# Kernel optimization log

Measured on AMD Instinct MI355X. Metric: run time of the kernel, lower is better.

## Reference

```python
import jax, jax.numpy as jnp
from jax import lax
import numpy as np

TAU = 10.0      # tauSr == tauRef
THR = 1.0       # theta
WIDTH = 1.0     # tauRho (surrogate width)
SCALE = 1.0     # scaleRho (surrogate scale)
DECAY = float(np.exp(-1.0 / TAU))


@jax.custom_vjp
def _heaviside(v):
    # spike = 1[v >= theta]
    return (v >= THR).astype(v.dtype)

def _heaviside_fwd(v):
    return _heaviside(v), v

def _heaviside_bwd(v, g):
    # SLAYER exponential surrogate pdf: scaleRho/tauRho * exp(-|v-theta|/tauRho)
    return (g * (SCALE / WIDTH) * jnp.exp(-jnp.abs(v - THR) / WIDTH),)

_heaviside.defvjp(_heaviside_fwd, _heaviside_bwd)


def _conv2d(x, w, pad):
    # x: (B, Cin, H, W), w: (Cout, Cin, kh, kw); SLAYER convs have no bias
    return lax.conv_general_dilated(
        x, w, window_strides=(1, 1), padding=[(pad, pad), (pad, pad)],
        dimension_numbers=("NCHW", "OIHW", "NCHW"))


def _sumpool(x, k):
    # SLAYER pool = sum over kxk window (times a learned scalar applied outside)
    B, C, H, W = x.shape
    return x.reshape(B, C, H // k, k, W // k, k).sum(axis=(3, 5))


def _psp(seq):
    # exponential synaptic (PSP) filter along time: s[t] = a*s[t-1] + x[t]
    a = jnp.asarray(DECAY, seq.dtype)
    def step(s, x_t):
        s = a * s + x_t
        return s, s
    _, out = lax.scan(step, jnp.zeros_like(seq[0]), seq)
    return out  # (T, ...)


def _spikes(u):
    # thresholded spiking with decaying refractory feedback (scaleRef=1):
    # v[t] = u[t] - r[t]; s[t] = 1[v >= theta]; r[t+1] = b*(r[t] + theta*s[t])
    b = jnp.asarray(DECAY, u.dtype)
    def step(r, u_t):
        s = _heaviside(u_t - r)
        r_next = b * (r + THR * s)
        return r_next, s
    _, out = lax.scan(step, jnp.zeros_like(u[0]), u)
    return out  # (T, ...)


def _forward(x, conv1_w, conv2_w, lin_w, w_pool1, w_pool2):
    N, T, C, H, W = x.shape  # (64, 100, 2, 32, 32)
    h = _conv2d(x.reshape(N * T, C, H, W), conv1_w, 2)        # (NT, 4, 32, 32)
    h = _sumpool(h, 4) * w_pool1                               # (NT, 4, 8, 8)
    h = h.reshape(N, T, 4, 8, 8).swapaxes(0, 1)                # (T, N, 4, 8, 8)
    s1 = _spikes(_psp(h))                                      # (T, N, 4, 8, 8)
    h2 = _conv2d(s1.reshape(T * N, 4, 8, 8), conv2_w, 1)       # (TN, 8, 8, 8)
    h2 = (_sumpool(h2, 2) * w_pool2).reshape(T, N, 8, 4, 4)    # (T, N, 8, 4, 4)
    s2 = _spikes(_psp(h2))                                     # (T, N, 8, 4, 4)
    # dense = full-spatial conv (2, 8, 4, 4) -> (N, T, 2)
    return jnp.einsum("tnchw,ochw->nto", s2, lin_w)


def setup_inputs() -> dict:
    key = jax.random.key(0)
    ks = jax.random.split(key, 4)
    x = (jax.random.uniform(ks[0], (64, 100, 2, 32, 32)) < 0.1).astype(jnp.float32)
    conv1_w = jax.random.normal(ks[1], (4, 2, 5, 5), jnp.float32) * 0.3
    conv2_w = jax.random.normal(ks[2], (8, 4, 3, 3), jnp.float32) * 0.3
    lin_w = jax.random.normal(ks[3], (2, 8, 4, 4), jnp.float32) * 0.3
    w_pool1 = jnp.float32(1.0 / 16.0)  # 1.1*theta / (16 * 1.1)
    w_pool2 = jnp.float32(1.0 / 4.0)   # 1.1*theta / (4 * 1.1)
    return {"x": x, "conv1_w": conv1_w, "conv2_w": conv2_w, "lin_w": lin_w,
            "w_pool1": w_pool1, "w_pool2": w_pool2}


def reference(x, conv1_w, conv2_w, lin_w, w_pool1, w_pool2):
    return _forward(x, conv1_w, conv2_w, lin_w, w_pool1, w_pool2)
```

## Files before the change

### kernel.cpp

```cpp
#include <hip/hip_runtime.h>


#define DECAY 0.9048374180359595f

#define BAR_LGKM() asm volatile("s_waitcnt lgkmcnt(0)\n\ts_barrier" ::: "memory")
#define FENCE_LGKM() asm volatile("s_waitcnt lgkmcnt(0)" ::: "memory")

typedef __attribute__((ext_vector_type(8))) _Float16 half8;

__global__ __launch_bounds__(128) void k0_fold(const float* __restrict__ w1,
        const float* __restrict__ w2, const float* __restrict__ wp1,
        const float* __restrict__ wp2, float* __restrict__ wl1,
        float* __restrict__ wl2, float* __restrict__ out) {
    const int tid = threadIdx.x;
    out[blockIdx.x * 128 + tid] = 0.f;
    if (blockIdx.x != 0) return;
    const float p1 = wp1[0], p2 = wp2[0];
    for (int idx = tid; idx < 512; idx += 128) {
        const int f = idx & 7, c = (idx >> 3) & 3, e = (idx >> 5) & 7, cin = idx >> 8;
        const int cc = c * 2 + cin;
        int alo = e - 3; if (alo < 0) alo = 0;
        int ahi = e;     if (ahi > 4) ahi = 4;
        int blo = f - 3; if (blo < 0) blo = 0;
        int bhi = f;     if (bhi > 4) bhi = 4;
        float s = 0.f;
        for (int a = alo; a <= ahi; ++a)
            for (int b = blo; b <= bhi; ++b)
                s += w1[cc * 25 + a * 5 + b];
        wl1[(cin * 8 + e) * 32 + c * 8 + f] = s * p1;
    }
    for (int idx = tid; idx < 512; idx += 128) {
        const int c2 = idx & 7, f = (idx >> 3) & 3, e = (idx >> 5) & 3, cin = idx >> 7;
        int alo = e - 1; if (alo < 0) alo = 0;
        int ahi = e;     if (ahi > 2) ahi = 2;
        int blo = f - 1; if (blo < 0) blo = 0;
        int bhi = f;     if (bhi > 2) bhi = 2;
        float s = 0.f;
        for (int aa = alo; aa <= ahi; ++aa)
            for (int bb = blo; bb <= bhi; ++bb)
                s += w2[((c2 * 4 + cin) * 3 + aa) * 3 + bb];
        wl2[c2 * 68 + cin * 16 + e * 4 + f] = s * p2;
    }
}

__global__ __launch_bounds__(64) void k1(const float* __restrict__ x,
        const float* __restrict__ wg, float* __restrict__ u1) {
    __shared__ __align__(16) float xs[2 * 1296];
    __shared__ __align__(16) float wl[512];
    const int lane = threadIdx.x;
    const int frame = blockIdx.x;
    const int n = frame / 100, t = frame % 100;

    *(float4*)(wl + 4 * lane)       = *(const float4*)(wg + 4 * lane);
    *(float4*)(wl + 256 + 4 * lane) = *(const float4*)(wg + 256 + 4 * lane);

    #pragma unroll
    for (int m0 = 0; m0 < 128; m0 += 64) {
        const int m = m0 + lane;
        if (m < 72) {
            const int cin = m / 36, rem = m % 36;
            const int rr = rem / 9, q4 = rem % 9;
            const int pr = (rr == 0) ? 0 : (rr == 1) ? 9 : (rr == 2) ? 26 : 35;
            *(float4*)(xs + cin * 1296 + pr * 36 + q4 * 4) = make_float4(0.f, 0.f, 0.f, 0.f);
        }
    }
    #pragma unroll
    for (int m0 = 0; m0 < 192; m0 += 64) {
        const int m = m0 + lane;
        if (m < 144) {
            const int cin = m / 72, rem = m % 72;
            const int side = rem & 1, pr = rem >> 1;
            *(float2*)(xs + cin * 1296 + pr * 36 + side * 34) = make_float2(0.f, 0.f);
        }
    }
    const float4* xg = (const float4*)(x + (size_t)frame * 2048);
    #pragma unroll
    for (int q = 0; q < 8; ++q) {
        const int m = q * 64 + lane;
        const float4 v = xg[m];
        const int li = 4 * m;
        const int cin = li >> 10, row = (li >> 5) & 31, col = li & 31;
        const int r = row + 2;
        const int pr = (r & 3) * 9 + (r >> 2);
        float* d = xs + cin * 1296 + pr * 36 + col + 2;
        *(float2*)(d)     = make_float2(v.x, v.y);
        *(float2*)(d + 2) = make_float2(v.z, v.w);
    }
    FENCE_LGKM();

    const int cp = lane >> 5;
    const int i  = (lane >> 2) & 7;
    const int jh = (lane >> 1) & 1;
    const int eh = lane & 1;

    float acc[2][4] = {{0.f, 0.f, 0.f, 0.f}, {0.f, 0.f, 0.f, 0.f}};
    const float* tb = xs + (i + eh) * 36 + jh * 16;
    #pragma unroll
    for (int cin = 0; cin < 2; ++cin) {
        #pragma unroll
        for (int et = 0; et < 4; ++et) {
            const int ro = cin * 1296 + et * 9 * 36;
            float xr[20];
            #pragma unroll
            for (int b = 0; b < 5; ++b)
                *(float4*)(xr + 4 * b) = *(const float4*)(tb + ro + 4 * b);
            float wv[16];
            const float* wp = wl + (cin * 8 + eh * 4 + et) * 32 + cp * 16;
            #pragma unroll
            for (int q = 0; q < 4; ++q)
                *(float4*)(wv + 4 * q) = *(const float4*)(wp + 4 * q);
            #pragma unroll
            for (int cl = 0; cl < 2; ++cl) {
                #pragma unroll
                for (int jj = 0; jj < 4; ++jj) {
                    const int o = 4 * jj;
                    acc[cl][jj] += xr[o]*wv[cl*8]     + xr[o+1]*wv[cl*8+1]
                                 + xr[o+2]*wv[cl*8+2] + xr[o+3]*wv[cl*8+3]
                                 + xr[o+4]*wv[cl*8+4] + xr[o+5]*wv[cl*8+5]
                                 + xr[o+6]*wv[cl*8+6] + xr[o+7]*wv[cl*8+7];
                }
            }
        }
    }
    #pragma unroll
    for (int cl = 0; cl < 2; ++cl)
        #pragma unroll
        for (int jj = 0; jj < 4; ++jj)
            acc[cl][jj] += __shfl_xor(acc[cl][jj], 1);

    const float o0 = eh ? acc[1][0] : acc[0][0];
    const float o1 = eh ? acc[1][1] : acc[0][1];
    const float o2 = eh ? acc[1][2] : acc[0][2];
    const float o3 = eh ? acc[1][3] : acc[0][3];
    *(float4*)(u1 + (size_t)t * 16384 + n * 256 + (2 * cp + eh) * 64 + i * 8 + jh * 4) =
        make_float4(o0, o1, o2, o3);
}

__global__ __launch_bounds__(256, 2) void kf(const float* __restrict__ u1,
        const float* __restrict__ wl2g, const float* __restrict__ lw,
        float* __restrict__ out) {
    __shared__ __align__(16) _Float16 ls1h[100 * 264];
    __shared__ __align__(16) float    ls2[100 * 20];
    const int tid = threadIdx.x;
    const int bid = blockIdx.x;
    const int n   = (bid & 7) * 8 + (bid >> 6);
    const int oct = (bid >> 3) & 7;
    const int wave = tid >> 6, l64 = tid & 63;
    const float a = DECAY;

    const float* up = u1 + n * 256 + tid;

    const int sub = tid >> 3, l8 = tid & 7;
    const int i2 = l8 >> 1, jhp = l8 & 1;

    float4 wreg[16];
    {
        const float* wbase = wl2g + oct * 68;
        #pragma unroll
        for (int q = 0; q < 16; ++q)
            wreg[q] = *(const float4*)(wbase + (q >> 2) * 16 + (q & 3) * 4);
    }

    float vbuf[100];
    #pragma unroll
    for (int k = 0; k < 100; ++k) vbuf[k] = up[(size_t)k * 16384];
    {
        float psp = 0.f, rr = 0.f;
        #pragma unroll
        for (int k = 0; k < 100; ++k) {
            psp = a * psp + vbuf[k];
            const float vv = psp - rr;
            const float s = (vv >= 1.f) ? 1.f : 0.f;
            rr = a * (rr + s);
            ls1h[k * 264 + tid] = (_Float16)s;
        }
    }
    BAR_LGKM();

    #pragma unroll 1
    for (int pass = 0; pass < 4; ++pass) {
        const int slot = sub + 32 * pass;
        if (slot < 100) {
            const _Float16* sb = ls1h + slot * 264;
            float acc0 = 0.f, acc1 = 0.f;
            #pragma unroll
            for (int cin = 0; cin < 4; ++cin) {
                #pragma unroll
                for (int e = 0; e < 4; ++e) {
                    const int ri = 2 * i2 + e - 1;
                    const int rc = (ri < 0) ? 0 : (ri > 7 ? 7 : ri);
                    const bool rok = (ri >= 0) && (ri <= 7);
                    const half8 hv = *(const half8*)(sb + cin * 64 + rc * 8);
                    float rr8[8];
                    #pragma unroll
                    for (int m = 0; m < 8; ++m) rr8[m] = (float)hv[m];
                    float xr[6];
                    xr[0] = jhp ? rr8[3] : 0.0f;
                    xr[1] = jhp ? rr8[4] : rr8[0];
                    xr[2] = jhp ? rr8[5] : rr8[1];
                    xr[3] = jhp ? rr8[6] : rr8[2];
                    xr[4] = jhp ? rr8[7] : rr8[3];
                    xr[5] = jhp ? 0.0f   : rr8[4];
                    if (!rok) {
                        #pragma unroll
                        for (int m = 0; m < 6; ++m) xr[m] = 0.0f;
                    }
                    const float4 wf = wreg[cin * 4 + e];
                    acc0 += xr[0] * wf.x; acc0 += xr[1] * wf.y;
                    acc0 += xr[2] * wf.z; acc0 += xr[3] * wf.w;
                    acc1 += xr[2] * wf.x; acc1 += xr[3] * wf.y;
                    acc1 += xr[4] * wf.z; acc1 += xr[5] * wf.w;
                }
            }
            *(float2*)(ls2 + slot * 20 + i2 * 4 + 2 * jhp) =
                make_float2(acc0, acc1);
        }
    }
    BAR_LGKM();

    if (wave == 0 && l64 < 16) {
        float ub[100];
        #pragma unroll
        for (int k = 0; k < 100; ++k) ub[k] = ls2[k * 20 + l64];
        float psp2 = 0.f, rr2 = 0.f;
        #pragma unroll
        for (int k = 0; k < 100; ++k) {
            psp2 = a * psp2 + ub[k];
            const float vv = psp2 - rr2;
            const float s = (vv >= 1.f) ? 1.f : 0.f;
            rr2 = a * (rr2 + s);
            ls2[k * 20 + l64] = s;
        }
    }
    BAR_LGKM();

    if (tid < 200) {
        const int t = tid >> 1, o = tid & 1;
        const float* srow = ls2 + t * 20;
        const float* wrow = lw + o * 128 + oct * 16;
        const float4 s0 = *(const float4*)(srow);
        const float4 s1 = *(const float4*)(srow + 4);
        const float4 s2 = *(const float4*)(srow + 8);
        const float4 s3 = *(const float4*)(srow + 12);
        const float4 w0 = *(const float4*)(wrow);
        const float4 w1 = *(const float4*)(wrow + 4);
        const float4 w2 = *(const float4*)(wrow + 8);
        const float4 w3 = *(const float4*)(wrow + 12);
        float v = 0.f;
        v += s0.x * w0.x; v += s0.y * w0.y; v += s0.z * w0.z; v += s0.w * w0.w;
        v += s1.x * w1.x; v += s1.y * w1.y; v += s1.z * w1.z; v += s1.w * w1.w;
        v += s2.x * w2.x; v += s2.y * w2.y; v += s2.z * w2.z; v += s2.w * w2.w;
        v += s3.x * w3.x; v += s3.y * w3.y; v += s3.z * w3.z; v += s3.w * w3.w;
        atomicAdd(&out[n * 200 + t * 2 + o], v);
    }
}

extern "C" void kernel_launch(void* const* d_in, const int* in_sizes, int n_in,
                              void* d_out, int out_size, void* d_ws, size_t ws_size,
                              hipStream_t stream) {
    const float* x   = (const float*)d_in[0];
    const float* w1  = (const float*)d_in[1];
    const float* w2  = (const float*)d_in[2];
    const float* lw  = (const float*)d_in[3];
    const float* wp1 = (const float*)d_in[4];
    const float* wp2 = (const float*)d_in[5];

    float* u1  = (float*)d_ws;
    float* wl1 = u1 + 1638400;
    float* wl2 = wl1 + 512;
    float* out = (float*)d_out;

    k0_fold<<<100, 128, 0, stream>>>(w1, w2, wp1, wp2, wl1, wl2, out);
    k1<<<6400, 64, 0, stream>>>(x, wl1, u1);
    kf<<<512, 256, 0, stream>>>(u1, wl2, lw, out);
}
```

Baseline: 117.6 us.

## Fuse weight folding, conv1 and recurrent stages into one cooperative kernel

Merges the three launches (weight fold, per-frame conv1, and the spiking/conv2/dense stage) into a single cooperative kernel of 512 blocks, separated by a grid-wide sync. Each block recomputes the folded conv1 and conv2 weights locally in shared memory, and its four waves each process one frame per pass over four passes. This removes launch overhead and the global workspace round trip for folded weights. In exchange it adds a grid barrier, caps the grid at 512 blocks for the conv1 phase, and raises shared memory use, which may limit occupancy.

Result: slower. 194.1 us (+65.0%).

```diff
diff --git a/kernel.cpp b/kernel.cpp
--- a/kernel.cpp
+++ b/kernel.cpp
@@ -1,4 +1,7 @@
 #include <hip/hip_runtime.h>
+#include <hip/hip_cooperative_groups.h>
+
+namespace cg = cooperative_groups;
 
 
 #define DECAY 0.9048374180359595f
@@ -8,29 +11,146 @@
 
 typedef __attribute__((ext_vector_type(8))) _Float16 half8;
 
-__global__ __launch_bounds__(128) void k0_fold(const float* __restrict__ w1,
-        const float* __restrict__ w2, const float* __restrict__ wp1,
-        const float* __restrict__ wp2, float* __restrict__ wl1,
-        float* __restrict__ wl2, float* __restrict__ out) {
-    const int tid = threadIdx.x;
-    out[blockIdx.x * 128 + tid] = 0.f;
-    if (blockIdx.x != 0) return;
-    const float p1 = wp1[0], p2 = wp2[0];
-    for (int idx = tid; idx < 512; idx += 128) {
-        const int f = idx & 7, c = (idx >> 3) & 3, e = (idx >> 5) & 7, cin = idx >> 8;
-        const int cc = c * 2 + cin;
-        int alo = e - 3; if (alo < 0) alo = 0;
-        int ahi = e;     if (ahi > 4) ahi = 4;
-        int blo = f - 3; if (blo < 0) blo = 0;
-        int bhi = f;     if (bhi > 4) bhi = 4;
-        float s = 0.f;
-        for (int a = alo; a <= ahi; ++a)
-            for (int b = blo; b <= bhi; ++b)
-                s += w1[cc * 25 + a * 5 + b];
-        wl1[(cin * 8 + e) * 32 + c * 8 + f] = s * p1;
-    }
-    for (int idx = tid; idx < 512; idx += 128) {
-        const int c2 = idx & 7, f = (idx >> 3) & 3, e = (idx >> 5) & 3, cin = idx >> 7;
+__global__ __launch_bounds__(256, 2) void kall(
+        const float* __restrict__ x,   const float* __restrict__ w1,
+        const float* __restrict__ w2,  const float* __restrict__ lw,
+        const float* __restrict__ wp1, const float* __restrict__ wp2,
+        float* __restrict__ u1,        float* __restrict__ out) {
+    __shared__ __align__(16) char smem[60800];
+    float*    xs_all = (float*)smem;
+    float*    wl1s   = (float*)(smem + 41472);
+    float*    w1s    = (float*)(smem + 43520);
+    _Float16* ls1h   = (_Float16*)smem;
+    float*    ls2    = (float*)(smem + 52800);
+
+    const int tid  = threadIdx.x;
+    const int bid  = blockIdx.x;
+    const int wave = tid >> 6, lane = tid & 63;
+    const float a = DECAY;
+
+    if (bid < 50) out[bid * 256 + tid] = 0.f;
+    if (tid < 200) w1s[tid] = w1[tid];
+    __syncthreads();
+    {
+        const float p1 = wp1[0];
+        #pragma unroll
+        for (int rep = 0; rep < 2; ++rep) {
+            const int idx = rep * 256 + tid;
+            const int f = idx & 7, c = (idx >> 3) & 3, e = (idx >> 5) & 7, cin = idx >> 8;
+            const int cc = c * 2 + cin;
+            int alo = e - 3; if (alo < 0) alo = 0;
+            int ahi = e;     if (ahi > 4) ahi = 4;
+            int blo = f - 3; if (blo < 0) blo = 0;
+            int bhi = f;     if (bhi > 4) bhi = 4;
+            float s = 0.f;
+            for (int aa = alo; aa <= ahi; ++aa)
+                for (int bb = blo; bb <= bhi; ++bb)
+                    s += w1s[cc * 25 + aa * 5 + bb];
+            wl1s[(cin * 8 + e) * 32 + c * 8 + f] = s * p1;
+        }
+    }
+    __syncthreads();
+
+    float* xs = xs_all + wave * 2592;
+    #pragma unroll 1
+    for (int pass = 0; pass < 4; ++pass) {
+        const int frame = pass * 2048 + bid * 4 + wave;
+        if (frame < 6400) {
+            const int n = frame / 100, t = frame % 100;
+
+            #pragma unroll
+            for (int m0 = 0; m0 < 128; m0 += 64) {
+                const int m = m0 + lane;
+                if (m < 72) {
+                    const int cin = m / 36, rem = m % 36;
+                    const int rr = rem / 9, q4 = rem % 9;
+                    const int pr = (rr == 0) ? 0 : (rr == 1) ? 9 : (rr == 2) ? 26 : 35;
+                    *(float4*)(xs + cin * 1296 + pr * 36 + q4 * 4) =
+                        make_float4(0.f, 0.f, 0.f, 0.f);
+                }
+            }
+            #pragma unroll
+            for (int m0 = 0; m0 < 192; m0 += 64) {
+                const int m = m0 + lane;
+                if (m < 144) {
+                    const int cin = m / 72, rem = m % 72;
+                    const int side = rem & 1, pr = rem >> 1;
+                    *(float2*)(xs + cin * 1296 + pr * 36 + side * 34) =
+                        make_float2(0.f, 0.f);
+                }
+            }
+            const float4* xg = (const float4*)(x + (size_t)frame * 2048);
+            #pragma unroll
+            for (int q = 0; q < 8; ++q) {
+                const int m = q * 64 + lane;
+                const float4 v = xg[m];
+                const int li = 4 * m;
+                const int cin = li >> 10, row = (li >> 5) & 31, col = li & 31;
+                const int r = row + 2;
+                const int pr = (r & 3) * 9 + (r >> 2);
+                float* d = xs + cin * 1296 + pr * 36 + col + 2;
+                *(float2*)(d)     = make_float2(v.x, v.y);
+                *(float2*)(d + 2) = make_float2(v.z, v.w);
+            }
+            FENCE_LGKM();
+
+            const int cp = lane >> 5;
+            const int i  = (lane >> 2) & 7;
+            const int jh = (lane >> 1) & 1;
+            const int eh = lane & 1;
+
+            float acc[2][4] = {{0.f, 0.f, 0.f, 0.f}, {0.f, 0.f, 0.f, 0.f}};
+            const float* tb = xs + (i + eh) * 36 + jh * 16;
+            #pragma unroll
+            for (int cin = 0; cin < 2; ++cin) {
+                #pragma unroll
+                for (int et = 0; et < 4; ++et) {
+                    const int ro = cin * 1296 + et * 9 * 36;
+                    float xr[20];
+                    #pragma unroll
+                    for (int b = 0; b < 5; ++b)
+                        *(float4*)(xr + 4 * b) = *(const float4*)(tb + ro + 4 * b);
+                    float wv[16];
+                    const float* wp = wl1s + (cin * 8 + eh * 4 + et) * 32 + cp * 16;
+                    #pragma unroll
+                    for (int q = 0; q < 4; ++q)
+                        *(float4*)(wv + 4 * q) = *(const float4*)(wp + 4 * q);
+                    #pragma unroll
+                    for (int cl = 0; cl < 2; ++cl) {
+                        #pragma unroll
+                        for (int jj = 0; jj < 4; ++jj) {
+                            const int o = 4 * jj;
+                            acc[cl][jj] += xr[o]*wv[cl*8]     + xr[o+1]*wv[cl*8+1]
+                                         + xr[o+2]*wv[cl*8+2] + xr[o+3]*wv[cl*8+3]
+                                         + xr[o+4]*wv[cl*8+4] + xr[o+5]*wv[cl*8+5]
+                                         + xr[o+6]*wv[cl*8+6] + xr[o+7]*wv[cl*8+7];
+                        }
+                    }
+                }
+            }
+            #pragma unroll
+            for (int cl = 0; cl < 2; ++cl)
+                #pragma unroll
+                for (int jj = 0; jj < 4; ++jj)
+                    acc[cl][jj] += __shfl_xor(acc[cl][jj], 1);
+
+            const float o0 = eh ? acc[1][0] : acc[0][0];
+            const float o1 = eh ? acc[1][1] : acc[0][1];
+            const float o2 = eh ? acc[1][2] : acc[0][2];
+            const float o3 = eh ? acc[1][3] : acc[0][3];
+            *(float4*)(u1 + (size_t)t * 16384 + n * 256 + (2 * cp + eh) * 64 + i * 8 + jh * 4) =
+                make_float4(o0, o1, o2, o3);
+        }
+    }
+
+    cg::this_grid().sync();
+
+    const int nB  = (bid & 7) * 8 + (bid >> 6);
+    const int oct = (bid >> 3) & 7;
+
+    if (tid < 64) {
+        const float p2 = wp2[0];
+        const int cin = tid >> 4, e = (tid >> 2) & 3, f = tid & 3;
         int alo = e - 1; if (alo < 0) alo = 0;
         int ahi = e;     if (ahi > 2) ahi = 2;
         int blo = f - 1; if (blo < 0) blo = 0;
@@ -38,128 +158,20 @@
         float s = 0.f;
         for (int aa = alo; aa <= ahi; ++aa)
             for (int bb = blo; bb <= bhi; ++bb)
-                s += w2[((c2 * 4 + cin) * 3 + aa) * 3 + bb];
-        wl2[c2 * 68 + cin * 16 + e * 4 + f] = s * p2;
-    }
-}
-
-__global__ __launch_bounds__(64) void k1(const float* __restrict__ x,
-        const float* __restrict__ wg, float* __restrict__ u1) {
-    __shared__ __align__(16) float xs[2 * 1296];
-    __shared__ __align__(16) float wl[512];
-    const int lane = threadIdx.x;
-    const int frame = blockIdx.x;
-    const int n = frame / 100, t = frame % 100;
-
-    *(float4*)(wl + 4 * lane)       = *(const float4*)(wg + 4 * lane);
-    *(float4*)(wl + 256 + 4 * lane) = *(const float4*)(wg + 256 + 4 * lane);
-
+                s += w2[((oct * 4 + cin) * 3 + aa) * 3 + bb];
+        ls2[cin * 16 + e * 4 + f] = s * p2;
+    }
+    __syncthreads();
+
+    float4 wreg[16];
     #pragma unroll
-    for (int m0 = 0; m0 < 128; m0 += 64) {
-        const int m = m0 + lane;
-        if (m < 72) {
-            const int cin = m / 36, rem = m % 36;
-            const int rr = rem / 9, q4 = rem % 9;
-            const int pr = (rr == 0) ? 0 : (rr == 1) ? 9 : (rr == 2) ? 26 : 35;
-            *(float4*)(xs + cin * 1296 + pr * 36 + q4 * 4) = make_float4(0.f, 0.f, 0.f, 0.f);
-        }
-    }
-    #pragma unroll
-    for (int m0 = 0; m0 < 192; m0 += 64) {
-        const int m = m0 + lane;
-        if (m < 144) {
-            const int cin = m / 72, rem = m % 72;
-            const int side = rem & 1, pr = rem >> 1;
-            *(float2*)(xs + cin * 1296 + pr * 36 + side * 34) = make_float2(0.f, 0.f);
-        }
-    }
-    const float4* xg = (const float4*)(x + (size_t)frame * 2048);
-    #pragma unroll
-    for (int q = 0; q < 8; ++q) {
-        const int m = q * 64 + lane;
-        const float4 v = xg[m];
-        const int li = 4 * m;
-        const int cin = li >> 10, row = (li >> 5) & 31, col = li & 31;
-        const int r = row + 2;
-        const int pr = (r & 3) * 9 + (r >> 2);
-        float* d = xs + cin * 1296 + pr * 36 + col + 2;
-        *(float2*)(d)     = make_float2(v.x, v.y);
-        *(float2*)(d + 2) = make_float2(v.z, v.w);
-    }
-    FENCE_LGKM();
-
-    const int cp = lane >> 5;
-    const int i  = (lane >> 2) & 7;
-    const int jh = (lane >> 1) & 1;
-    const int eh = lane & 1;
-
-    float acc[2][4] = {{0.f, 0.f, 0.f, 0.f}, {0.f, 0.f, 0.f, 0.f}};
-    const float* tb = xs + (i + eh) * 36 + jh * 16;
-    #pragma unroll
-    for (int cin = 0; cin < 2; ++cin) {
-        #pragma unroll
-        for (int et = 0; et < 4; ++et) {
-            const int ro = cin * 1296 + et * 9 * 36;
-            float xr[20];
-            #pragma unroll
-            for (int b = 0; b < 5; ++b)
-                *(float4*)(xr + 4 * b) = *(const float4*)(tb + ro + 4 * b);
-            float wv[16];
-            const float* wp = wl + (cin * 8 + eh * 4 + et) * 32 + cp * 16;
-            #pragma unroll
-            for (int q = 0; q < 4; ++q)
-                *(float4*)(wv + 4 * q) = *(const float4*)(wp + 4 * q);
-            #pragma unroll
-            for (int cl = 0; cl < 2; ++cl) {
-                #pragma unroll
-                for (int jj = 0; jj < 4; ++jj) {
-                    const int o = 4 * jj;
-                    acc[cl][jj] += xr[o]*wv[cl*8]     + xr[o+1]*wv[cl*8+1]
-                                 + xr[o+2]*wv[cl*8+2] + xr[o+3]*wv[cl*8+3]
-                                 + xr[o+4]*wv[cl*8+4] + xr[o+5]*wv[cl*8+5]
-                                 + xr[o+6]*wv[cl*8+6] + xr[o+7]*wv[cl*8+7];
-                }
-            }
-        }
-    }
-    #pragma unroll
-    for (int cl = 0; cl < 2; ++cl)
-        #pragma unroll
-        for (int jj = 0; jj < 4; ++jj)
-            acc[cl][jj] += __shfl_xor(acc[cl][jj], 1);
-
-    const float o0 = eh ? acc[1][0] : acc[0][0];
-    const float o1 = eh ? acc[1][1] : acc[0][1];
-    const float o2 = eh ? acc[1][2] : acc[0][2];
-    const float o3 = eh ? acc[1][3] : acc[0][3];
-    *(float4*)(u1 + (size_t)t * 16384 + n * 256 + (2 * cp + eh) * 64 + i * 8 + jh * 4) =
-        make_float4(o0, o1, o2, o3);
-}
-
-__global__ __launch_bounds__(256, 2) void kf(const float* __restrict__ u1,
-        const float* __restrict__ wl2g, const float* __restrict__ lw,
-        float* __restrict__ out) {
-    __shared__ __align__(16) _Float16 ls1h[100 * 264];
-    __shared__ __align__(16) float    ls2[100 * 20];
-    const int tid = threadIdx.x;
-    const int bid = blockIdx.x;
-    const int n   = (bid & 7) * 8 + (bid >> 6);
-    const int oct = (bid >> 3) & 7;
-    const int wave = tid >> 6, l64 = tid & 63;
-    const float a = DECAY;
-
-    const float* up = u1 + n * 256 + tid;
+    for (int q = 0; q < 16; ++q)
+        wreg[q] = *(const float4*)(ls2 + (q >> 2) * 16 + (q & 3) * 4);
+
+    const float* up = u1 + nB * 256 + tid;
 
     const int sub = tid >> 3, l8 = tid & 7;
     const int i2 = l8 >> 1, jhp = l8 & 1;
-
-    float4 wreg[16];
-    {
-        const float* wbase = wl2g + oct * 68;
-        #pragma unroll
-        for (int q = 0; q < 16; ++q)
-            wreg[q] = *(const float4*)(wbase + (q >> 2) * 16 + (q & 3) * 4);
-    }
 
     float vbuf[100];
     #pragma unroll
@@ -218,10 +230,11 @@
     }
     BAR_LGKM();
 
-    if (wave == 0 && l64 < 16) {
+    if (wave == 0 && (tid & 63) < 16) {
+        const int cell = tid & 63;
         float ub[100];
         #pragma unroll
-        for (int k = 0; k < 100; ++k) ub[k] = ls2[k * 20 + l64];
+        for (int k = 0; k < 100; ++k) ub[k] = ls2[k * 20 + cell];
         float psp2 = 0.f, rr2 = 0.f;
         #pragma unroll
         for (int k = 0; k < 100; ++k) {
@@ -229,7 +242,7 @@
             const float vv = psp2 - rr2;
             const float s = (vv >= 1.f) ? 1.f : 0.f;
             rr2 = a * (rr2 + s);
-            ls2[k * 20 + l64] = s;
+            ls2[k * 20 + cell] = s;
         }
     }
     BAR_LGKM();
@@ -243,15 +256,15 @@
         const float4 s2 = *(const float4*)(srow + 8);
         const float4 s3 = *(const float4*)(srow + 12);
         const float4 w0 = *(const float4*)(wrow);
-        const float4 w1 = *(const float4*)(wrow + 4);
-        const float4 w2 = *(const float4*)(wrow + 8);
+        const float4 w1v = *(const float4*)(wrow + 4);
+        const float4 w2v = *(const float4*)(wrow + 8);
         const float4 w3 = *(const float4*)(wrow + 12);
         float v = 0.f;
-        v += s0.x * w0.x; v += s0.y * w0.y; v += s0.z * w0.z; v += s0.w * w0.w;
-        v += s1.x * w1.x; v += s1.y * w1.y; v += s1.z * w1.z; v += s1.w * w1.w;
-        v += s2.x * w2.x; v += s2.y * w2.y; v += s2.z * w2.z; v += s2.w * w2.w;
-        v += s3.x * w3.x; v += s3.y * w3.y; v += s3.z * w3.z; v += s3.w * w3.w;
-        atomicAdd(&out[n * 200 + t * 2 + o], v);
+        v += s0.x * w0.x;  v += s0.y * w0.y;  v += s0.z * w0.z;  v += s0.w * w0.w;
+        v += s1.x * w1v.x; v += s1.y * w1v.y; v += s1.z * w1v.z; v += s1.w * w1v.w;
+        v += s2.x * w2v.x; v += s2.y * w2v.y; v += s2.z * w2v.z; v += s2.w * w2v.w;
+        v += s3.x * w3.x;  v += s3.y * w3.y;  v += s3.z * w3.z;  v += s3.w * w3.w;
+        atomicAdd(&out[nB * 200 + t * 2 + o], v);
     }
 }
 
@@ -266,11 +279,10 @@
     const float* wp2 = (const float*)d_in[5];
 
     float* u1  = (float*)d_ws;
-    float* wl1 = u1 + 1638400;
-    float* wl2 = wl1 + 512;
     float* out = (float*)d_out;
 
-    k0_fold<<<100, 128, 0, stream>>>(w1, w2, wp1, wp2, wl1, wl2, out);
-    k1<<<6400, 64, 0, stream>>>(x, wl1, u1);
-    kf<<<512, 256, 0, stream>>>(u1, wl2, lw, out);
+    void* args[] = { (void*)&x, (void*)&w1, (void*)&w2, (void*)&lw,
+                     (void*)&wp1, (void*)&wp2, (void*)&u1, (void*)&out };
+    hipLaunchCooperativeKernel((const void*)kall, dim3(512), dim3(256),
+                               args, 0, stream);
 }
```

## Stream u1 time series through double-buffered LDS via global_load_lds

Applied to the files above, without the earlier changes.

Replaces the 100-register prefetch of the u1 time series with a double-buffered LDS pipeline that uses global_load_lds, loading chunks of 8 timesteps while the PSP/spike recurrence consumes the previous chunk. The goal is to free about 100 VGPRs per thread, which should help occupancy under the 256x2 launch bound, and to overlap global loads with the serial recurrence. In exchange it adds 16 KB of LDS per block, manual vmcnt accounting that must match the number of issued loads, and a serial 13-step loop with waits that may expose memory latency.

New measurement: 124.1 us. +5.5%, slower.

```diff
diff --git a/kernel.cpp b/kernel.cpp
--- a/kernel.cpp
+++ b/kernel.cpp
@@ -7,6 +7,10 @@
 #define FENCE_LGKM() asm volatile("s_waitcnt lgkmcnt(0)" ::: "memory")
 
 typedef __attribute__((ext_vector_type(8))) _Float16 half8;
+
+#define GLOAD_LDS4(gp, lp) __builtin_amdgcn_global_load_lds(                    \
+    (const __attribute__((address_space(1))) void*)(gp),                        \
+    (__attribute__((address_space(3))) void*)(lp), 4, 0, 0)
 
 __global__ __launch_bounds__(128) void k0_fold(const float* __restrict__ w1,
         const float* __restrict__ w2, const float* __restrict__ wp1,
@@ -140,6 +144,7 @@
         const float* __restrict__ wl2g, const float* __restrict__ lw,
         float* __restrict__ out) {
     __shared__ __align__(16) _Float16 ls1h[100 * 264];
+    __shared__ __align__(16) float    ubuf[2][8 * 256];
     __shared__ __align__(16) float    ls2[100 * 20];
     const int tid = threadIdx.x;
     const int bid = blockIdx.x;
@@ -148,8 +153,6 @@
     const int wave = tid >> 6, l64 = tid & 63;
     const float a = DECAY;
 
-    const float* up = u1 + n * 256 + tid;
-
     const int sub = tid >> 3, l8 = tid & 7;
     const int i2 = l8 >> 1, jhp = l8 & 1;
 
@@ -160,19 +163,50 @@
         for (int q = 0; q < 16; ++q)
             wreg[q] = *(const float4*)(wbase + (q >> 2) * 16 + (q & 3) * 4);
     }
-
-    float vbuf[100];
-    #pragma unroll
-    for (int k = 0; k < 100; ++k) vbuf[k] = up[(size_t)k * 16384];
+    asm volatile("s_waitcnt vmcnt(0)" ::: "memory");
+
     {
+        const float* usrc = u1 + n * 256 + tid;
+        float* const wbase0 = &ubuf[0][wave * 64];
+        float* const wbase1 = &ubuf[1][wave * 64];
+
+        #pragma unroll
+        for (int kk = 0; kk < 8; ++kk)
+            GLOAD_LDS4(usrc + (size_t)kk * 16384, wbase0 + kk * 256);
+
         float psp = 0.f, rr = 0.f;
-        #pragma unroll
-        for (int k = 0; k < 100; ++k) {
-            psp = a * psp + vbuf[k];
-            const float vv = psp - rr;
-            const float s = (vv >= 1.f) ? 1.f : 0.f;
-            rr = a * (rr + s);
-            ls1h[k * 264 + tid] = (_Float16)s;
+        #pragma unroll 1
+        for (int c = 0; c < 13; ++c) {
+            if (c < 11) {
+                float* const dst = ((c + 1) & 1) ? wbase1 : wbase0;
+                const int kb = (c + 1) * 8;
+                #pragma unroll
+                for (int kk = 0; kk < 8; ++kk)
+                    GLOAD_LDS4(usrc + (size_t)(kb + kk) * 16384, dst + kk * 256);
+            } else if (c == 11) {
+                float* const dst = wbase0;
+                #pragma unroll
+                for (int kk = 0; kk < 4; ++kk)
+                    GLOAD_LDS4(usrc + (size_t)(96 + kk) * 16384, dst + kk * 256);
+            }
+            if (c < 11)      asm volatile("s_waitcnt vmcnt(8)" ::: "memory");
+            else if (c < 12) asm volatile("s_waitcnt vmcnt(4)" ::: "memory");
+            else             asm volatile("s_waitcnt vmcnt(0)" ::: "memory");
+            __builtin_amdgcn_sched_barrier(0);
+
+            const float* src = (c & 1) ? &ubuf[1][0] : &ubuf[0][0];
+            const int cnt = (c == 12) ? 4 : 8;
+            #pragma unroll
+            for (int kk = 0; kk < 8; ++kk) {
+                if (kk < cnt) {
+                    const float v = src[kk * 256 + tid];
+                    psp = a * psp + v;
+                    const float vv = psp - rr;
+                    const float s = (vv >= 1.f) ? 1.f : 0.f;
+                    rr = a * (rr + s);
+                    ls1h[(c * 8 + kk) * 264 + tid] = (_Float16)s;
+                }
+            }
         }
     }
     BAR_LGKM();
```
